# Kernel tuning notes

Hardware: AMD Instinct MI355X
Metric: run time of the kernel (lower is better)

## Reference

```python
import jax, jax.numpy as jnp
import numpy as np

D = 1024
N_HEAD = 16
D_HEAD = D // N_HEAD


def setup_inputs() -> dict:
    key = jax.random.key(0)
    k1, k2, k3 = jax.random.split(key, 3)
    x = jax.random.normal(k1, (4, 2048, D), dtype=jnp.float32)
    # torch nn.Linear weights: [out_features, in_features]
    W_qkv = jax.random.normal(k2, (3 * D, D), dtype=jnp.float32) * (1.0 / np.sqrt(D))
    W_o = jax.random.normal(k3, (D, D), dtype=jnp.float32) * (1.0 / np.sqrt(D))
    return {"x": x, "W_qkv": W_qkv, "W_o": W_o}


def reference(x, W_qkv, W_o):
    b, s, d = x.shape
    qkv = x @ W_qkv.T                      # [b, s, 3d]
    q, k, v = jnp.split(qkv, 3, axis=-1)
    # [b, s, d] -> [b, h, s, dh]
    def heads(z):
        return z.reshape(b, s, N_HEAD, D_HEAD).transpose(0, 2, 1, 3)
    q, k, v = heads(q), heads(k), heads(v)
    scores = jnp.einsum("bhqd,bhkd->bhqk", q, k) / np.sqrt(D_HEAD).astype(np.float32)
    causal = jnp.tril(jnp.ones((s, s), dtype=bool))  # True = keep
    scores = jnp.where(causal, scores, -jnp.inf)
    attn = jax.nn.softmax(scores, axis=-1)
    out = jnp.einsum("bhqk,bhkd->bhqd", attn, v)     # [b, h, s, dh]
    out = out.transpose(0, 2, 1, 3).reshape(b, s, d)
    return out @ W_o.T
```

## Files before the change

### kernel.cpp

```cpp
#include <hip/hip_runtime.h>


typedef _Float16 f16x8 __attribute__((ext_vector_type(8)));
typedef __fp16 fp16x2 __attribute__((ext_vector_type(2)));
typedef float floatx4 __attribute__((ext_vector_type(4)));
typedef unsigned int uint2v __attribute__((ext_vector_type(2)));

union U4H8 { uint4 u; f16x8 h; };

__device__ __forceinline__ ushort f32_to_h_bits(float f) {
  _Float16 h = (_Float16)f;
  return __builtin_bit_cast(ushort, h);
}
__device__ __forceinline__ uint pack2h(float a, float b) {
  return (uint)f32_to_h_bits(a) | ((uint)f32_to_h_bits(b) << 16);
}
__device__ __forceinline__ uint pkrtz(float a, float b) {
  fp16x2 r = __builtin_amdgcn_cvt_pkrtz(a, b);
  return __builtin_bit_cast(uint, r);
}
__device__ __forceinline__ float exp2_fast(float x) {
  float r;
  asm("v_exp_f32 %0, %1" : "=v"(r) : "v"(x));
  return r;
}

__device__ __forceinline__ uint4 qtrans(uint pA, uint pB, uint pC, uint pD) {
  uint2v ac = __builtin_amdgcn_permlane32_swap(pA, pC, false, false);
  uint2v bd = __builtin_amdgcn_permlane32_swap(pB, pD, false, false);
  uint2v ac2 = __builtin_amdgcn_permlane16_swap(ac[0], ac[1], false, false);
  uint2v bd2 = __builtin_amdgcn_permlane16_swap(bd[0], bd[1], false, false);
  return (uint4){ac2[0], bd2[0], ac2[1], bd2[1]};
}

__device__ __forceinline__ void gld16(const void* g, void* l) {
  __builtin_amdgcn_global_load_lds(
      (const __attribute__((address_space(1))) unsigned char*)g,
      (__attribute__((address_space(3))) unsigned char*)l, 16, 0, 0);
}

__global__ __launch_bounds__(256) void cast_f32_f16(const float* __restrict__ in,
                                                    ushort* __restrict__ out) {
  int i = blockIdx.x * 256 + threadIdx.x;
  float4 v = ((const float4*)in)[i];
  ushort4 o;
  o.x = f32_to_h_bits(v.x);
  o.y = f32_to_h_bits(v.y);
  o.z = f32_to_h_bits(v.z);
  o.w = f32_to_h_bits(v.w);
  ((ushort4*)out)[i] = o;
}

template <int OUT_F16>
__global__ __launch_bounds__(256) void gemm_bt(const ushort* __restrict__ A,
                                               const ushort* __restrict__ B,
                                               void* __restrict__ Cv,
                                               int M, int N, int K) {
  __shared__ ushort As[3][4096];
  __shared__ ushort Bs[3][4096];

  const int tid = threadIdx.x;
  const int lane = tid & 63;
  const int w = tid >> 6;
  const int l15 = lane & 15;
  const int quad = lane >> 4;

  const int gx = gridDim.x;
  const int lin = blockIdx.y * gx + blockIdx.x;
  const int qq = (gx * gridDim.y) >> 3;
  const int nl = (lin & 7) * qq + (lin >> 3);
  const int m0 = (nl / gx) * 128;
  const int n0 = (nl % gx) * 128;

  const int wm = (w & 1) * 64;
  const int wn = (w >> 1) * 64;

  floatx4 acc[4][4];
#pragma unroll
  for (int i = 0; i < 4; i++)
#pragma unroll
    for (int j = 0; j < 4; j++) acc[i][j] = (floatx4){0.f, 0.f, 0.f, 0.f};

  const int srow = w * 16 + (lane >> 2);
  const int sq = ((lane & 3) ^ ((lane >> 3) & 3)) * 8;
  const ushort* Ap = A + (size_t)(m0 + srow) * K + sq;
  const ushort* Bp = B + (size_t)(n0 + srow) * K + sq;
  const size_t rstep = (size_t)64 * K;

  auto stage = [&](int k0, int buf) {
    gld16(Ap + k0, &As[buf][w * 512]);
    gld16(Ap + rstep + k0, &As[buf][(w + 4) * 512]);
    gld16(Bp + k0, &Bs[buf][w * 512]);
    gld16(Bp + rstep + k0, &Bs[buf][(w + 4) * 512]);
  };

  stage(0, 0);
  stage(32, 1);

  const int psw = (quad ^ ((l15 >> 1) & 3)) * 8;

  int bt = 0;
  int bs = 2;
  for (int k0 = 0; k0 < K; k0 += 32) {
    if (k0 + 64 < K) {
      asm volatile("s_waitcnt vmcnt(4)" ::: "memory");
    } else {
      asm volatile("s_waitcnt vmcnt(0)" ::: "memory");
    }
    __builtin_amdgcn_s_barrier();
    asm volatile("" ::: "memory");
    if (k0 + 64 < K) stage(k0 + 64, bs);

    U4H8 af[4], bf[4];
#pragma unroll
    for (int mi = 0; mi < 4; mi++)
      af[mi].u = *(const uint4*)&As[bt][(wm + mi * 16 + l15) * 32 + psw];
#pragma unroll
    for (int ni = 0; ni < 4; ni++)
      bf[ni].u = *(const uint4*)&Bs[bt][(wn + ni * 16 + l15) * 32 + psw];
#pragma unroll
    for (int mi = 0; mi < 4; mi++)
#pragma unroll
      for (int ni = 0; ni < 4; ni++)
        acc[mi][ni] = __builtin_amdgcn_mfma_f32_16x16x32_f16(af[mi].h, bf[ni].h,
                                                             acc[mi][ni], 0, 0, 0);
    bt = (bt == 2) ? 0 : bt + 1;
    bs = (bs == 2) ? 0 : bs + 1;
  }

#pragma unroll
  for (int mi = 0; mi < 4; mi++) {
#pragma unroll
    for (int r = 0; r < 4; r++) {
      size_t row = m0 + wm + mi * 16 + quad * 4 + r;
#pragma unroll
      for (int ni = 0; ni < 4; ni++) {
        size_t col = n0 + wn + ni * 16 + l15;
        float v = acc[mi][ni][r];
        if (OUT_F16)
          ((ushort*)Cv)[row * N + col] = f32_to_h_bits(v);
        else
          ((float*)Cv)[row * N + col] = v;
      }
    }
  }
}

__global__ __launch_bounds__(256) void vtrans(const ushort* __restrict__ qkv,
                                              ushort* __restrict__ vtg) {
  __shared__ ushort T[64 * 66];
  const int tid = threadIdx.x;
  const int kt = blockIdx.x;
  const int bh = blockIdx.y;
  const int b = bh >> 4, h = bh & 15;

  const int r = tid >> 3;
  const int c = (tid & 7) * 8;
  const ushort* src = qkv + (size_t)(b * 2048 + kt * 64) * 3072 + 2048 + h * 64;
  uint4 v0 = *(const uint4*)(src + (size_t)r * 3072 + c);
  uint4 v1 = *(const uint4*)(src + (size_t)(r + 32) * 3072 + c);
  union { uint4 u; ushort s[8]; } a0, a1;
  a0.u = v0; a1.u = v1;
#pragma unroll
  for (int j = 0; j < 8; j++) {
    T[(c + j) * 66 + r] = a0.s[j];
    T[(c + j) * 66 + r + 32] = a1.s[j];
  }
  __syncthreads();

  const int d = tid >> 3;
  const int kc = (tid & 7) * 8;
  ushort* dst = vtg + (size_t)bh * 64 * 2048 + (size_t)kt * 64;
  union { uint u[4]; uint4 u4; } o0, o1;
#pragma unroll
  for (int i = 0; i < 4; i++) {
    o0.u[i] = *(const uint*)&T[d * 66 + kc + 2 * i];
    o1.u[i] = *(const uint*)&T[(d + 32) * 66 + kc + 2 * i];
  }
  *(uint4*)(dst + (size_t)d * 2048 + kc) = o0.u4;
  *(uint4*)(dst + (size_t)(d + 32) * 2048 + kc) = o1.u4;
}

__global__ __launch_bounds__(256, 4) void attn_fused(const ushort* __restrict__ qkv,
                                                     const ushort* __restrict__ vtg,
                                                     ushort* __restrict__ attn_out) {
  __shared__ ushort Ks[2][4096];
  __shared__ ushort Vs[2][4096];

  const int tid = threadIdx.x;
  const int lane = tid & 63;
  const int w = tid >> 6;
  const int l15 = lane & 15;
  const int quad = lane >> 4;
  const int id = blockIdx.x;
  const int n_ = id >> 3;
  const int bx = n_ >> 3;
  const int bh = (id & 7) * 8 + (n_ & 7);
  const int b = bh >> 4;
  const int h = bh & 15;
  const int bS = b * 2048;
  const int qtA = bx;
  const int qtB = 31 - bx;
  const int ktmax = qtB;
  const int q0A = qtA * 64 + w * 16;
  const int q0B = qtB * 64 + w * 16;

  U4H8 qf0[2], qf1[2];
  {
    const ushort* qrowA = qkv + (size_t)(bS + q0A + l15) * 3072 + h * 64;
    const ushort* qrowB = qkv + (size_t)(bS + q0B + l15) * 3072 + h * 64;
#pragma unroll
    for (int kc = 0; kc < 2; kc++) {
      qf0[kc].u = *(const uint4*)(qrowA + kc * 32 + quad * 8);
      qf0[kc].h = qf0[kc].h * (_Float16)0.1803368787f;
      qf1[kc].u = *(const uint4*)(qrowB + kc * 32 + quad * 8);
      qf1[kc].h = qf1[kc].h * (_Float16)0.1803368787f;
    }
  }

  floatx4 o0[4], o1[4];
#pragma unroll
  for (int ni = 0; ni < 4; ni++) {
    o0[ni] = (floatx4){0.f, 0.f, 0.f, 0.f};
    o1[ni] = (floatx4){0.f, 0.f, 0.f, 0.f};
  }
  float m0v = -1e30f, m1v = -1e30f, l0v = 0.f, l1v = 0.f;

  const ushort* kbase = qkv + (size_t)bS * 3072 + 1024 + h * 64;
  const ushort* vbase = vtg + (size_t)bh * 64 * 2048;
  const int sr = lane & 15;
  const int scc = (lane >> 4) * 8;

  auto stage = [&](int kt, int buf) {
    const ushort* kg = kbase + (size_t)(kt * 64 + w * 16 + sr) * 3072 + scc;
    gld16(kg, &Ks[buf][(w * 2 + 0) * 512]);
    gld16(kg + 32, &Ks[buf][(w * 2 + 1) * 512]);
    const ushort* vg = vbase + (size_t)(w * 16 + sr) * 2048 + (size_t)kt * 64 + scc;
    gld16(vg, &Vs[buf][(w * 2 + 0) * 512]);
    gld16(vg + 32, &Vs[buf][(w * 2 + 1) * 512]);
  };

  stage(0, 0);
  for (int kt = 0; kt <= ktmax; ++kt) {
    const int buf = kt & 1;
    __syncthreads();
    if (kt < ktmax) stage(kt + 1, buf ^ 1);
    const bool dual = (kt <= qtA);
    const int kt64 = kt * 64;

    floatx4 s1[4], s0[4];
    __builtin_amdgcn_s_setprio(1);
#pragma unroll
    for (int t = 0; t < 4; t++) {
      U4H8 kf0, kf1;
      kf0.u = *(const uint4*)&Ks[buf][(t * 2 + 0) * 512 + lane * 8];
      kf1.u = *(const uint4*)&Ks[buf][(t * 2 + 1) * 512 + lane * 8];
      floatx4 a = (floatx4){0.f, 0.f, 0.f, 0.f};
      a = __builtin_amdgcn_mfma_f32_16x16x32_f16(kf0.h, qf1[0].h, a, 0, 0, 0);
      a = __builtin_amdgcn_mfma_f32_16x16x32_f16(kf1.h, qf1[1].h, a, 0, 0, 0);
      s1[t] = a;
      if (dual) {
        floatx4 c = (floatx4){0.f, 0.f, 0.f, 0.f};
        c = __builtin_amdgcn_mfma_f32_16x16x32_f16(kf0.h, qf0[0].h, c, 0, 0, 0);
        c = __builtin_amdgcn_mfma_f32_16x16x32_f16(kf1.h, qf0[1].h, c, 0, 0, 0);
        s0[t] = c;
      }
    }
    __builtin_amdgcn_s_setprio(0);

    if (kt == qtB) {
      const int q = q0B + l15;
#pragma unroll
      for (int t = 0; t < 4; t++)
#pragma unroll
        for (int r = 0; r < 4; r++) {
          int key = kt64 + t * 16 + quad * 4 + r;
          if (key > q) s1[t][r] = -1e30f;
        }
    }
    if (dual && kt == qtA) {
      const int q = q0A + l15;
#pragma unroll
      for (int t = 0; t < 4; t++)
#pragma unroll
        for (int r = 0; r < 4; r++) {
          int key = kt64 + t * 16 + quad * 4 + r;
          if (key > q) s0[t][r] = -1e30f;
        }
    }

    {
      float a1 = fmaxf(fmaxf(s1[0][0], s1[0][1]), fmaxf(s1[0][2], s1[0][3]));
      float b1 = fmaxf(fmaxf(s1[1][0], s1[1][1]), fmaxf(s1[1][2], s1[1][3]));
      float c1 = fmaxf(fmaxf(s1[2][0], s1[2][1]), fmaxf(s1[2][2], s1[2][3]));
      float d1 = fmaxf(fmaxf(s1[3][0], s1[3][1]), fmaxf(s1[3][2], s1[3][3]));
      float t1 = fmaxf(fmaxf(a1, b1), fmaxf(c1, d1));
      t1 = fmaxf(t1, __shfl_xor(t1, 16));
      t1 = fmaxf(t1, __shfl_xor(t1, 32));
      if (__any(t1 > m1v)) {
        float mnew = fmaxf(m1v, t1);
        float alpha = exp2_fast(m1v - mnew);
        m1v = mnew;
        l1v *= alpha;
#pragma unroll
        for (int ni = 0; ni < 4; ni++) o1[ni] *= alpha;
      }
      float rs1 = 0.f;
#pragma unroll
      for (int t = 0; t < 4; t++)
#pragma unroll
        for (int r = 0; r < 4; r++) {
          float p = exp2_fast(s1[t][r] - m1v);
          s1[t][r] = p;
          rs1 += p;
        }
      rs1 += __shfl_xor(rs1, 16);
      rs1 += __shfl_xor(rs1, 32);
      l1v += rs1;
    }
    if (dual) {
      float a0 = fmaxf(fmaxf(s0[0][0], s0[0][1]), fmaxf(s0[0][2], s0[0][3]));
      float b0 = fmaxf(fmaxf(s0[1][0], s0[1][1]), fmaxf(s0[1][2], s0[1][3]));
      float c0 = fmaxf(fmaxf(s0[2][0], s0[2][1]), fmaxf(s0[2][2], s0[2][3]));
      float d0 = fmaxf(fmaxf(s0[3][0], s0[3][1]), fmaxf(s0[3][2], s0[3][3]));
      float t0 = fmaxf(fmaxf(a0, b0), fmaxf(c0, d0));
      t0 = fmaxf(t0, __shfl_xor(t0, 16));
      t0 = fmaxf(t0, __shfl_xor(t0, 32));
      if (__any(t0 > m0v)) {
        float mnew = fmaxf(m0v, t0);
        float alpha = exp2_fast(m0v - mnew);
        m0v = mnew;
        l0v *= alpha;
#pragma unroll
        for (int ni = 0; ni < 4; ni++) o0[ni] *= alpha;
      }
      float rs0 = 0.f;
#pragma unroll
      for (int t = 0; t < 4; t++)
#pragma unroll
        for (int r = 0; r < 4; r++) {
          float p = exp2_fast(s0[t][r] - m0v);
          s0[t][r] = p;
          rs0 += p;
        }
      rs0 += __shfl_xor(rs0, 16);
      rs0 += __shfl_xor(rs0, 32);
      l0v += rs0;
    }

#pragma unroll
    for (int kc = 0; kc < 2; kc++) {
      U4H8 pb1, pb0;
      pb1.u = qtrans(pkrtz(s1[kc * 2][0], s1[kc * 2][1]),
                     pkrtz(s1[kc * 2][2], s1[kc * 2][3]),
                     pkrtz(s1[kc * 2 + 1][0], s1[kc * 2 + 1][1]),
                     pkrtz(s1[kc * 2 + 1][2], s1[kc * 2 + 1][3]));
      if (dual)
        pb0.u = qtrans(pkrtz(s0[kc * 2][0], s0[kc * 2][1]),
                       pkrtz(s0[kc * 2][2], s0[kc * 2][3]),
                       pkrtz(s0[kc * 2 + 1][0], s0[kc * 2 + 1][1]),
                       pkrtz(s0[kc * 2 + 1][2], s0[kc * 2 + 1][3]));
      __builtin_amdgcn_s_setprio(1);
#pragma unroll
      for (int ni = 0; ni < 4; ni++) {
        U4H8 vf;
        vf.u = *(const uint4*)&Vs[buf][(ni * 2 + kc) * 512 + lane * 8];
        o1[ni] = __builtin_amdgcn_mfma_f32_16x16x32_f16(vf.h, pb1.h, o1[ni], 0, 0, 0);
        if (dual)
          o0[ni] = __builtin_amdgcn_mfma_f32_16x16x32_f16(vf.h, pb0.h, o0[ni], 0, 0, 0);
      }
      __builtin_amdgcn_s_setprio(0);
    }
  }

  {
    float inv = 1.0f / l1v;
    ushort* orow = attn_out + (size_t)(bS + q0B + l15) * 1024 + h * 64;
#pragma unroll
    for (int p = 0; p < 2; p++) {
      uint4 x = qtrans(pack2h(o1[p * 2][0] * inv, o1[p * 2][1] * inv),
                       pack2h(o1[p * 2][2] * inv, o1[p * 2][3] * inv),
                       pack2h(o1[p * 2 + 1][0] * inv, o1[p * 2 + 1][1] * inv),
                       pack2h(o1[p * 2 + 1][2] * inv, o1[p * 2 + 1][3] * inv));
      *(uint4*)(orow + p * 32 + quad * 8) = x;
    }
  }
  {
    float inv = 1.0f / l0v;
    ushort* orow = attn_out + (size_t)(bS + q0A + l15) * 1024 + h * 64;
#pragma unroll
    for (int p = 0; p < 2; p++) {
      uint4 x = qtrans(pack2h(o0[p * 2][0] * inv, o0[p * 2][1] * inv),
                       pack2h(o0[p * 2][2] * inv, o0[p * 2][3] * inv),
                       pack2h(o0[p * 2 + 1][0] * inv, o0[p * 2 + 1][1] * inv),
                       pack2h(o0[p * 2 + 1][2] * inv, o0[p * 2 + 1][3] * inv));
      *(uint4*)(orow + p * 32 + quad * 8) = x;
    }
  }
}

extern "C" void kernel_launch(void* const* d_in, const int* in_sizes, int n_in,
                              void* d_out, int out_size, void* d_ws, size_t ws_size,
                              hipStream_t stream) {
  const float* x = (const float*)d_in[0];
  const float* wqkv = (const float*)d_in[1];
  const float* wo = (const float*)d_in[2];
  float* out = (float*)d_out;

  ushort* xh = (ushort*)d_ws;
  ushort* wqkvh = xh + (size_t)8192 * 1024;
  ushort* woh = wqkvh + (size_t)3072 * 1024;
  ushort* qkvh = woh + (size_t)1024 * 1024;
  ushort* attnh = qkvh + (size_t)8192 * 3072;
  ushort* vtg = attnh + (size_t)8192 * 1024;

  cast_f32_f16<<<8192, 256, 0, stream>>>(x, xh);
  cast_f32_f16<<<3072, 256, 0, stream>>>(wqkv, wqkvh);
  cast_f32_f16<<<1024, 256, 0, stream>>>(wo, woh);

  gemm_bt<1><<<dim3(24, 64), 256, 0, stream>>>(xh, wqkvh, qkvh, 8192, 3072, 1024);
  vtrans<<<dim3(32, 64), 256, 0, stream>>>(qkvh, vtg);
  attn_fused<<<dim3(1024), 256, 0, stream>>>(qkvh, vtg, attnh);
  gemm_bt<0><<<dim3(8, 64), 256, 0, stream>>>(attnh, woh, out, 8192, 1024, 1024);
}
```

Baseline: 262.6 us.

## Split dual-tile attention loop into two sequential passes per query tile

```diff
diff --git a/kernel.cpp b/kernel.cpp
--- a/kernel.cpp
+++ b/kernel.cpp
@@ -180,6 +180,72 @@
   *(uint4*)(dst + (size_t)d * 2048 + kc) = o0.u4;
   *(uint4*)(dst + (size_t)(d + 32) * 2048 + kc) = o1.u4;
 }
+
+#define ATTN_STEP(QF, Q0V, MV, LV, OA, KT64, BUF, DIAG)                        \
+  do {                                                                         \
+    floatx4 ss[4];                                                             \
+    __builtin_amdgcn_s_setprio(1);                                             \
+    _Pragma("unroll") for (int t = 0; t < 4; t++) {                            \
+      U4H8 kfa, kfb;                                                           \
+      kfa.u = *(const uint4*)&Ks[BUF][(t * 2 + 0) * 512 + lane * 8];           \
+      kfb.u = *(const uint4*)&Ks[BUF][(t * 2 + 1) * 512 + lane * 8];           \
+      floatx4 aa = (floatx4){0.f, 0.f, 0.f, 0.f};                              \
+      aa = __builtin_amdgcn_mfma_f32_16x16x32_f16(kfa.h, QF[0].h, aa, 0, 0, 0);\
+      aa = __builtin_amdgcn_mfma_f32_16x16x32_f16(kfb.h, QF[1].h, aa, 0, 0, 0);\
+      ss[t] = aa;                                                              \
+    }                                                                          \
+    __builtin_amdgcn_s_setprio(0);                                             \
+    if (DIAG) {                                                                \
+      const int qv = (Q0V) + l15;                                              \
+      _Pragma("unroll") for (int t = 0; t < 4; t++)                            \
+          _Pragma("unroll") for (int r = 0; r < 4; r++) {                      \
+        int key = (KT64) + t * 16 + quad * 4 + r;                              \
+        if (key > qv) ss[t][r] = -1e30f;                                       \
+      }                                                                        \
+    }                                                                          \
+    float fa = fmaxf(fmaxf(ss[0][0], ss[0][1]), fmaxf(ss[0][2], ss[0][3]));    \
+    float fb = fmaxf(fmaxf(ss[1][0], ss[1][1]), fmaxf(ss[1][2], ss[1][3]));    \
+    float fc = fmaxf(fmaxf(ss[2][0], ss[2][1]), fmaxf(ss[2][2], ss[2][3]));    \
+    float fd = fmaxf(fmaxf(ss[3][0], ss[3][1]), fmaxf(ss[3][2], ss[3][3]));    \
+    float tm = fmaxf(fmaxf(fa, fb), fmaxf(fc, fd));                            \
+    tm = fmaxf(tm, __shfl_xor(tm, 16));                                        \
+    tm = fmaxf(tm, __shfl_xor(tm, 32));                                        \
+    if (__any(tm > (MV))) {                                                    \
+      float mnew = fmaxf((MV), tm);                                            \
+      float alpha = exp2_fast((MV)-mnew);                                      \
+      (MV) = mnew;                                                             \
+      (LV) *= alpha;                                                           \
+      _Pragma("unroll") for (int ni = 0; ni < 4; ni++) OA[ni] *= alpha;        \
+    }                                                                          \
+    {                                                                          \
+      const float mm = (MV);                                                   \
+      float rs = 0.f;                                                          \
+      _Pragma("unroll") for (int t = 0; t < 4; t++)                            \
+          _Pragma("unroll") for (int r = 0; r < 4; r++) {                      \
+        float p = exp2_fast(ss[t][r] - mm);                                    \
+        ss[t][r] = p;                                                          \
+        rs += p;                                                               \
+      }                                                                        \
+      rs += __shfl_xor(rs, 16);                                                \
+      rs += __shfl_xor(rs, 32);                                                \
+      (LV) += rs;                                                              \
+    }                                                                          \
+    _Pragma("unroll") for (int kc = 0; kc < 2; kc++) {                         \
+      U4H8 pb;                                                                 \
+      pb.u = qtrans(pkrtz(ss[kc * 2][0], ss[kc * 2][1]),                       \
+                    pkrtz(ss[kc * 2][2], ss[kc * 2][3]),                       \
+                    pkrtz(ss[kc * 2 + 1][0], ss[kc * 2 + 1][1]),               \
+                    pkrtz(ss[kc * 2 + 1][2], ss[kc * 2 + 1][3]));              \
+      __builtin_amdgcn_s_setprio(1);                                           \
+      _Pragma("unroll") for (int ni = 0; ni < 4; ni++) {                       \
+        U4H8 vf;                                                               \
+        vf.u = *(const uint4*)&Vs[BUF][(ni * 2 + kc) * 512 + lane * 8];        \
+        OA[ni] =                                                               \
+            __builtin_amdgcn_mfma_f32_16x16x32_f16(vf.h, pb.h, OA[ni], 0, 0, 0);\
+      }                                                                        \
+      __builtin_amdgcn_s_setprio(0);                                           \
+    }                                                                          \
+  } while (0)
 
 __global__ __launch_bounds__(256, 4) void attn_fused(const ushort* __restrict__ qkv,
                                                      const ushort* __restrict__ vtg,
@@ -201,7 +267,6 @@
   const int bS = b * 2048;
   const int qtA = bx;
   const int qtB = 31 - bx;
-  const int ktmax = qtB;
   const int q0A = qtA * 64 + w * 16;
   const int q0B = qtB * 64 + w * 16;
 
@@ -241,136 +306,18 @@
   };
 
   stage(0, 0);
-  for (int kt = 0; kt <= ktmax; ++kt) {
-    const int buf = kt & 1;
+  int u = 0;
+  for (int kt = 0; kt <= qtB; ++kt, ++u) {
+    const int buf = u & 1;
     __syncthreads();
-    if (kt < ktmax) stage(kt + 1, buf ^ 1);
-    const bool dual = (kt <= qtA);
-    const int kt64 = kt * 64;
-
-    floatx4 s1[4], s0[4];
-    __builtin_amdgcn_s_setprio(1);
-#pragma unroll
-    for (int t = 0; t < 4; t++) {
-      U4H8 kf0, kf1;
-      kf0.u = *(const uint4*)&Ks[buf][(t * 2 + 0) * 512 + lane * 8];
-      kf1.u = *(const uint4*)&Ks[buf][(t * 2 + 1) * 512 + lane * 8];
-      floatx4 a = (floatx4){0.f, 0.f, 0.f, 0.f};
-      a = __builtin_amdgcn_mfma_f32_16x16x32_f16(kf0.h, qf1[0].h, a, 0, 0, 0);
-      a = __builtin_amdgcn_mfma_f32_16x16x32_f16(kf1.h, qf1[1].h, a, 0, 0, 0);
-      s1[t] = a;
-      if (dual) {
-        floatx4 c = (floatx4){0.f, 0.f, 0.f, 0.f};
-        c = __builtin_amdgcn_mfma_f32_16x16x32_f16(kf0.h, qf0[0].h, c, 0, 0, 0);
-        c = __builtin_amdgcn_mfma_f32_16x16x32_f16(kf1.h, qf0[1].h, c, 0, 0, 0);
-        s0[t] = c;
-      }
-    }
-    __builtin_amdgcn_s_setprio(0);
-
-    if (kt == qtB) {
-      const int q = q0B + l15;
-#pragma unroll
-      for (int t = 0; t < 4; t++)
-#pragma unroll
-        for (int r = 0; r < 4; r++) {
-          int key = kt64 + t * 16 + quad * 4 + r;
-          if (key > q) s1[t][r] = -1e30f;
-        }
-    }
-    if (dual && kt == qtA) {
-      const int q = q0A + l15;
-#pragma unroll
-      for (int t = 0; t < 4; t++)
-#pragma unroll
-        for (int r = 0; r < 4; r++) {
-          int key = kt64 + t * 16 + quad * 4 + r;
-          if (key > q) s0[t][r] = -1e30f;
-        }
-    }
-
-    {
-      float a1 = fmaxf(fmaxf(s1[0][0], s1[0][1]), fmaxf(s1[0][2], s1[0][3]));
-      float b1 = fmaxf(fmaxf(s1[1][0], s1[1][1]), fmaxf(s1[1][2], s1[1][3]));
-      float c1 = fmaxf(fmaxf(s1[2][0], s1[2][1]), fmaxf(s1[2][2], s1[2][3]));
-      float d1 = fmaxf(fmaxf(s1[3][0], s1[3][1]), fmaxf(s1[3][2], s1[3][3]));
-      float t1 = fmaxf(fmaxf(a1, b1), fmaxf(c1, d1));
-      t1 = fmaxf(t1, __shfl_xor(t1, 16));
-      t1 = fmaxf(t1, __shfl_xor(t1, 32));
-      if (__any(t1 > m1v)) {
-        float mnew = fmaxf(m1v, t1);
-        float alpha = exp2_fast(m1v - mnew);
-        m1v = mnew;
-        l1v *= alpha;
-#pragma unroll
-        for (int ni = 0; ni < 4; ni++) o1[ni] *= alpha;
-      }
-      float rs1 = 0.f;
-#pragma unroll
-      for (int t = 0; t < 4; t++)
-#pragma unroll
-        for (int r = 0; r < 4; r++) {
-          float p = exp2_fast(s1[t][r] - m1v);
-          s1[t][r] = p;
-          rs1 += p;
-        }
-      rs1 += __shfl_xor(rs1, 16);
-      rs1 += __shfl_xor(rs1, 32);
-      l1v += rs1;
-    }
-    if (dual) {
-      float a0 = fmaxf(fmaxf(s0[0][0], s0[0][1]), fmaxf(s0[0][2], s0[0][3]));
-      float b0 = fmaxf(fmaxf(s0[1][0], s0[1][1]), fmaxf(s0[1][2], s0[1][3]));
-      float c0 = fmaxf(fmaxf(s0[2][0], s0[2][1]), fmaxf(s0[2][2], s0[2][3]));
-      float d0 = fmaxf(fmaxf(s0[3][0], s0[3][1]), fmaxf(s0[3][2], s0[3][3]));
-      float t0 = fmaxf(fmaxf(a0, b0), fmaxf(c0, d0));
-      t0 = fmaxf(t0, __shfl_xor(t0, 16));
-      t0 = fmaxf(t0, __shfl_xor(t0, 32));
-      if (__any(t0 > m0v)) {
-        float mnew = fmaxf(m0v, t0);
-        float alpha = exp2_fast(m0v - mnew);
-        m0v = mnew;
-        l0v *= alpha;
-#pragma unroll
-        for (int ni = 0; ni < 4; ni++) o0[ni] *= alpha;
-      }
-      float rs0 = 0.f;
-#pragma unroll
-      for (int t = 0; t < 4; t++)
-#pragma unroll
-        for (int r = 0; r < 4; r++) {
-          float p = exp2_fast(s0[t][r] - m0v);
-          s0[t][r] = p;
-          rs0 += p;
-        }
-      rs0 += __shfl_xor(rs0, 16);
-      rs0 += __shfl_xor(rs0, 32);
-      l0v += rs0;
-    }
-
-#pragma unroll
-    for (int kc = 0; kc < 2; kc++) {
-      U4H8 pb1, pb0;
-      pb1.u = qtrans(pkrtz(s1[kc * 2][0], s1[kc * 2][1]),
-                     pkrtz(s1[kc * 2][2], s1[kc * 2][3]),
-                     pkrtz(s1[kc * 2 + 1][0], s1[kc * 2 + 1][1]),
-                     pkrtz(s1[kc * 2 + 1][2], s1[kc * 2 + 1][3]));
-      if (dual)
-        pb0.u = qtrans(pkrtz(s0[kc * 2][0], s0[kc * 2][1]),
-                       pkrtz(s0[kc * 2][2], s0[kc * 2][3]),
-                       pkrtz(s0[kc * 2 + 1][0], s0[kc * 2 + 1][1]),
-                       pkrtz(s0[kc * 2 + 1][2], s0[kc * 2 + 1][3]));
-      __builtin_amdgcn_s_setprio(1);
-#pragma unroll
-      for (int ni = 0; ni < 4; ni++) {
-        U4H8 vf;
-        vf.u = *(const uint4*)&Vs[buf][(ni * 2 + kc) * 512 + lane * 8];
-        o1[ni] = __builtin_amdgcn_mfma_f32_16x16x32_f16(vf.h, pb1.h, o1[ni], 0, 0, 0);
-        if (dual)
-          o0[ni] = __builtin_amdgcn_mfma_f32_16x16x32_f16(vf.h, pb0.h, o0[ni], 0, 0, 0);
-      }
-      __builtin_amdgcn_s_setprio(0);
-    }
+    stage(kt < qtB ? kt + 1 : 0, buf ^ 1);
+    ATTN_STEP(qf1, q0B, m1v, l1v, o1, kt * 64, buf, kt == qtB);
+  }
+  for (int kt = 0; kt <= qtA; ++kt, ++u) {
+    const int buf = u & 1;
+    __syncthreads();
+    if (kt < qtA) stage(kt + 1, buf ^ 1);
+    ATTN_STEP(qf0, q0A, m0v, l0v, o0, kt * 64, buf, kt == qtA);
   }
 
   {
```

Result: no change. 262.7 us (+0.1%).
